# Kernel optimization log

Measured on AMD Instinct MI355X. Metric: run time of the kernel, lower is better.

The kernel has to match this reference:

```python
import jax, jax.numpy as jnp
import numpy as np


def setup_inputs() -> dict:
    key = jax.random.key(0)
    ks = jax.random.split(key, 10)
    B, S, H, I, V = 64, 2048, 512, 512, 50257
    scale = 0.05
    return {
        "last_output": jax.random.randint(ks[0], (B,), 0, V),
        "last_hidden": jax.random.normal(ks[1], (1, B, H), jnp.float32),
        "encoder_outputs": jax.random.normal(ks[2], (S, B, H), jnp.float32),
        "embedding": jax.random.normal(ks[3], (V, I), jnp.float32) * scale,
        "W_ih": jax.random.normal(ks[4], (3 * H, I + H), jnp.float32) * scale,
        "b_ih": jax.random.normal(ks[5], (3 * H,), jnp.float32) * scale,
        "W_hh": jax.random.normal(ks[6], (3 * H, H), jnp.float32) * scale,
        "b_hh": jax.random.normal(ks[7], (3 * H,), jnp.float32) * scale,
        "W_out": jax.random.normal(ks[8], (V, 2 * H), jnp.float32) * scale,
        "b_out": jax.random.normal(ks[9], (V,), jnp.float32) * scale,
    }


def _gru_step(x, h, W_ih, b_ih, W_hh, b_hh):
    # torch nn.GRU parametrization, single layer, single timestep.
    H = h.shape[-1]
    gi = x @ W_ih.T + b_ih  # [B, 3H]
    gh = h @ W_hh.T + b_hh  # [B, 3H]
    i_r, i_z, i_n = gi[:, :H], gi[:, H:2 * H], gi[:, 2 * H:]
    h_r, h_z, h_n = gh[:, :H], gh[:, H:2 * H], gh[:, 2 * H:]
    r = jax.nn.sigmoid(i_r + h_r)
    z = jax.nn.sigmoid(i_z + h_z)
    n = jnp.tanh(i_n + r * h_n)
    return (1.0 - z) * n + z * h


def reference(last_output, last_hidden, encoder_outputs, embedding,
              W_ih, b_ih, W_hh, b_hh, W_out, b_out):
    # Embedding lookup: [B, I]
    embedded = embedding[last_output]
    h_top = last_hidden[-1]  # [B, H]
    # Luong 'dot' attention: score(b, s) = h_b . enc[s, b]
    scores = jnp.einsum('bh,sbh->bs', h_top, encoder_outputs)  # [B, S]
    attn = jax.nn.softmax(scores, axis=-1)                      # [B, S]
    # context = attn @ enc (per batch): [B, H]
    context = jnp.einsum('bs,sbh->bh', attn, encoder_outputs)
    # GRU single step on cat(embedded, context)
    rnn_in = jnp.concatenate([embedded, context], axis=-1)      # [B, I+H]
    h_new = _gru_step(rnn_in, h_top, W_ih, b_ih, W_hh, b_hh)    # [B, H]
    # Output projection on cat(rnn_out, context) -> log_softmax over vocab
    feat = jnp.concatenate([h_new, context], axis=-1)           # [B, 2H]
    logits = feat @ W_out.T + b_out                             # [B, V]
    logp = jax.nn.log_softmax(logits, axis=-1)
    hidden = h_new[None]  # [1, B, H]
    return logp, hidden
```

## Files before the change

### kernel.cpp

```cpp
#include <hip/hip_runtime.h>
#include <hip/hip_bf16.h>
#include <math.h>

#define BB 64
#define SS 2048
#define HH 512
#define VV 50257
#define KD 1024
#define NSPLIT 32
#define NTILE 786

typedef float f32x4 __attribute__((ext_vector_type(4)));
typedef __bf16 bf16x8 __attribute__((ext_vector_type(8)));
typedef __attribute__((address_space(3))) void lds_void;
typedef __attribute__((address_space(1))) const void glb_void;

__device__ __forceinline__ float dot4(float4 a, float4 b) {
  return a.x*b.x + a.y*b.y + a.z*b.z + a.w*b.w;
}

__device__ __forceinline__ bf16x8 cvt8(float4 a, float4 b) {
  bf16x8 r;
  r[0]=(__bf16)a.x; r[1]=(__bf16)a.y; r[2]=(__bf16)a.z; r[3]=(__bf16)a.w;
  r[4]=(__bf16)b.x; r[5]=(__bf16)b.y; r[6]=(__bf16)b.z; r[7]=(__bf16)b.w;
  return r;
}

__device__ __forceinline__ size_t fragAddr(int b, int k) {
  return (size_t)(k >> 5)*2048 + (size_t)(b >> 4)*512
       + (size_t)((k >> 3) & 3)*128 + (size_t)(b & 15)*8 + (size_t)(k & 7);
}

__global__ __launch_bounds__(256) void attn_partial(
    const float* __restrict__ hprev, const float* __restrict__ enc,
    float* __restrict__ pm, float* __restrict__ pl, float* __restrict__ pacc)
{
  const int b = blockIdx.x >> 5;
  const int split = blockIdx.x & 31;
  const int t = threadIdx.x;
  const int w = t >> 6, lane = t & 63;

  const float* hb = hprev + b*HH + lane*8;
  const float4 h0 = *(const float4*)hb;
  const float4 h1 = *(const float4*)(hb + 4);
  const int s0 = split*64 + w*16;

  float m = -INFINITY, lsum = 0.f;
  float acc[8];
#pragma unroll
  for (int j = 0; j < 8; ++j) acc[j] = 0.f;

#pragma unroll 1
  for (int half = 0; half < 2; ++half) {
    float4 ea[8], eb[8];
#pragma unroll
    for (int i = 0; i < 8; ++i) {
      const float* ep = enc + ((size_t)(s0 + half*8 + i)*BB + b)*HH + lane*8;
      ea[i] = *(const float4*)ep; eb[i] = *(const float4*)(ep + 4);
    }
    float dd[8];
#pragma unroll
    for (int i = 0; i < 8; ++i) dd[i] = dot4(h0, ea[i]) + dot4(h1, eb[i]);
#pragma unroll
    for (int off = 32; off >= 1; off >>= 1) {
#pragma unroll
      for (int i = 0; i < 8; ++i) dd[i] += __shfl_xor(dd[i], off, 64);
    }
    float hm = dd[0];
#pragma unroll
    for (int i = 1; i < 8; ++i) hm = fmaxf(hm, dd[i]);
    const float mn = fmaxf(m, hm);
    const float sc = __expf(m - mn);
    float p[8], psum = 0.f;
#pragma unroll
    for (int i = 0; i < 8; ++i) { p[i] = __expf(dd[i] - mn); psum += p[i]; }
    lsum = lsum*sc + psum;
#pragma unroll
    for (int j = 0; j < 8; ++j) acc[j] *= sc;
#pragma unroll
    for (int i = 0; i < 8; ++i) {
      acc[0] += p[i]*ea[i].x; acc[1] += p[i]*ea[i].y;
      acc[2] += p[i]*ea[i].z; acc[3] += p[i]*ea[i].w;
      acc[4] += p[i]*eb[i].x; acc[5] += p[i]*eb[i].y;
      acc[6] += p[i]*eb[i].z; acc[7] += p[i]*eb[i].w;
    }
    m = mn;
  }

  __shared__ float sm4[4], sl4[4];
  __shared__ float sacc[4][HH];
  if (lane == 0) { sm4[w] = m; sl4[w] = lsum; }
  __syncthreads();
  const float M = fmaxf(fmaxf(sm4[0], sm4[1]), fmaxf(sm4[2], sm4[3]));
  const float ew = __expf(m - M);
#pragma unroll
  for (int j = 0; j < 8; ++j) sacc[w][lane*8 + j] = acc[j]*ew;
  __syncthreads();

  const int rec = blockIdx.x;
  for (int hh = t; hh < HH; hh += 256)
    pacc[(size_t)rec*HH + hh] = sacc[0][hh]+sacc[1][hh]+sacc[2][hh]+sacc[3][hh];
  if (t == 0) {
    float L = sl4[0]*__expf(sm4[0]-M) + sl4[1]*__expf(sm4[1]-M)
            + sl4[2]*__expf(sm4[2]-M) + sl4[3]*__expf(sm4[3]-M);
    pm[rec] = M; pl[rec] = L;
  }
}

__global__ __launch_bounds__(256) void attn_reduce(
    const float* __restrict__ pm, const float* __restrict__ pl,
    const float* __restrict__ pacc, __hip_bfloat16* __restrict__ featA)
{
  const int b = blockIdx.x, t = threadIdx.x;
  __shared__ float smm[NSPLIT], sll[NSPLIT], sco[NSPLIT];
  if (t < NSPLIT) { smm[t] = pm[b*NSPLIT + t]; sll[t] = pl[b*NSPLIT + t]; }
  __syncthreads();
  float M = -INFINITY;
  for (int q = 0; q < NSPLIT; ++q) M = fmaxf(M, smm[q]);
  float L = 0.f;
  for (int q = 0; q < NSPLIT; ++q) L += sll[q]*__expf(smm[q]-M);
  const float inv = 1.f/L;
  if (t < NSPLIT) sco[t] = __expf(smm[t]-M)*inv;
  __syncthreads();
  const int hh0 = 2*t;
  float s0 = 0.f, s1 = 0.f;
  for (int q = 0; q < NSPLIT; ++q) {
    const float* pq = pacc + ((size_t)b*NSPLIT + q)*HH;
    s0 += pq[hh0]   * sco[q];
    s1 += pq[hh0+1] * sco[q];
  }
  const size_t a = fragAddr(b, HH + hh0);
  featA[a]   = (__hip_bfloat16)s0;
  featA[a+1] = (__hip_bfloat16)s1;
}

__global__ __launch_bounds__(256) void gru_gemm(
    const int* __restrict__ last_out, const float* __restrict__ emb,
    const float* __restrict__ hprev, const __hip_bfloat16* __restrict__ featA,
    const float* __restrict__ W_ih, const float* __restrict__ W_hh,
    float* __restrict__ gates)
{
  const int u = blockIdx.x;
  const int gt = u / 12;
  const int rem = u % 12;
  const int seg = rem >> 2, ks = rem & 3;
  const int w = threadIdx.x >> 6, lane = threadIdx.x & 63;
  const int col = lane & 15, kg = lane >> 4;
  const int g = gt*64 + w*16 + col;

  const float* wrow = (seg == 2) ? (W_hh + (size_t)g*HH)
                                 : (W_ih + (size_t)g*KD + seg*HH);
  int lo_r[4];
#pragma unroll
  for (int mt = 0; mt < 4; ++mt) lo_r[mt] = last_out[mt*16 + col];

  f32x4 acc[4];
#pragma unroll
  for (int mt = 0; mt < 4; ++mt) acc[mt] = (f32x4){0.f,0.f,0.f,0.f};

  const int kbeg = ks*128, kend = kbeg + 128;
  for (int k0 = kbeg; k0 < kend; k0 += 32) {
    const float* wp = wrow + k0 + kg*8;
    const bf16x8 bf = cvt8(*(const float4*)wp, *(const float4*)(wp+4));
#pragma unroll
    for (int mt = 0; mt < 4; ++mt) {
      const int bb = mt*16 + col;
      bf16x8 af;
      if (seg == 0) {
        const float* ap = emb + (size_t)lo_r[mt]*HH + k0 + kg*8;
        af = cvt8(*(const float4*)ap, *(const float4*)(ap+4));
      } else if (seg == 1) {
        af = *(const bf16x8*)(featA + fragAddr(bb, HH + k0 + kg*8));
      } else {
        const float* ap = hprev + (size_t)bb*HH + k0 + kg*8;
        af = cvt8(*(const float4*)ap, *(const float4*)(ap+4));
      }
      acc[mt] = __builtin_amdgcn_mfma_f32_16x16x32_bf16(af, bf, acc[mt], 0, 0, 0);
    }
  }

  float* gp = gates + (size_t)rem*BB*1536;
#pragma unroll
  for (int mt = 0; mt < 4; ++mt)
#pragma unroll
    for (int reg = 0; reg < 4; ++reg) {
      const int brow = mt*16 + kg*4 + reg;
      gp[(size_t)brow*1536 + g] = acc[mt][reg];
    }
}

__global__ __launch_bounds__(512) void gru_pointwise(
    const float* __restrict__ gates, const float* __restrict__ hprev,
    const float* __restrict__ b_ih, const float* __restrict__ b_hh,
    float* __restrict__ hid_out, __hip_bfloat16* __restrict__ featA)
{
  const int b = blockIdx.x, j = threadIdx.x;

  float i_r = 0.f, i_z = 0.f, i_n = 0.f;
#pragma unroll
  for (int p = 0; p < 8; ++p) {
    const float* gp = gates + ((size_t)p*BB + b)*1536;
    i_r += gp[j]; i_z += gp[HH + j]; i_n += gp[2*HH + j];
  }
  float h_r = 0.f, h_z = 0.f, h_n = 0.f;
#pragma unroll
  for (int p = 8; p < 12; ++p) {
    const float* gp = gates + ((size_t)p*BB + b)*1536;
    h_r += gp[j]; h_z += gp[HH + j]; h_n += gp[2*HH + j];
  }

  const float r = 1.f/(1.f + __expf(-(i_r + h_r + b_ih[j] + b_hh[j])));
  const float z = 1.f/(1.f + __expf(-(i_z + h_z + b_ih[HH+j] + b_hh[HH+j])));
  const float n = tanhf(i_n + b_ih[2*HH+j] + r*(h_n + b_hh[2*HH+j]));
  const float hp = hprev[b*HH + j];
  const float hn = (1.f - z)*n + z*hp;
  hid_out[b*HH + j] = hn;
  featA[fragAddr(b, j)] = (__hip_bfloat16)hn;
}

__global__ __launch_bounds__(256, 6) void logits_gemm(
    const __hip_bfloat16* __restrict__ featA, const float* __restrict__ W_out,
    const float* __restrict__ b_out, float* __restrict__ out,
    float* __restrict__ pmE, float* __restrict__ plE)
{
  __shared__ float smem[4672];
  const int tile = blockIdx.x;
  const int t = threadIdx.x;
  const int w = t >> 6, lane = t & 63;
  const int col = lane & 15, kg = lane >> 4;
  const int vbase = tile*64;
  const int v = vbase + w*16 + col;
  const int rowL = w*16 + col;
  const int sXor = (rowL & 7) << 2;

  const __hip_bfloat16* fp = featA + lane*8;

  auto stage = [&](int buf, int kc) {
#pragma unroll
    for (int i = 0; i < 2; ++i) {
      const int sigma = (w*2 + i)*64 + lane;
      const int row = sigma >> 3;
      const int t16 = sigma & 7;
      const int kdl = (t16*4) ^ ((row & 7) << 2);
      int grow = vbase + row; if (grow > VV-1) grow = VV-1;
      const float* src = W_out + (size_t)grow*KD + kc*32 + kdl;
      __builtin_amdgcn_global_load_lds((glb_void*)src,
          (lds_void*)(smem + buf*2048 + (w*2 + i)*256), 16, 0, 0);
    }
  };

  f32x4 acc[4];
#pragma unroll
  for (int mt = 0; mt < 4; ++mt) acc[mt] = (f32x4){0.f,0.f,0.f,0.f};

  stage(0, 0);
  stage(1, 1);

#pragma unroll 1
  for (int kc = 0; kc < 32; ++kc) {
    if (kc < 31) asm volatile("s_waitcnt vmcnt(2)" ::: "memory");
    else         asm volatile("s_waitcnt vmcnt(0)" ::: "memory");
    __builtin_amdgcn_sched_barrier(0);
    __builtin_amdgcn_s_barrier();

    const float* wt = smem + (kc & 1)*2048;
    const int kin = kg*8;
    const float4 wa = *(const float4*)(wt + rowL*32 + (kin ^ sXor));
    const float4 wb = *(const float4*)(wt + rowL*32 + ((kin + 4) ^ sXor));
    const bf16x8 bf = cvt8(wa, wb);
    const __hip_bfloat16* f = fp + (size_t)kc*2048;
    acc[0] = __builtin_amdgcn_mfma_f32_16x16x32_bf16(*(const bf16x8*)(f),        bf, acc[0], 0, 0, 0);
    acc[1] = __builtin_amdgcn_mfma_f32_16x16x32_bf16(*(const bf16x8*)(f + 512),  bf, acc[1], 0, 0, 0);
    acc[2] = __builtin_amdgcn_mfma_f32_16x16x32_bf16(*(const bf16x8*)(f + 1024), bf, acc[2], 0, 0, 0);
    acc[3] = __builtin_amdgcn_mfma_f32_16x16x32_bf16(*(const bf16x8*)(f + 1536), bf, acc[3], 0, 0, 0);

    __builtin_amdgcn_s_barrier();
    if (kc + 2 < 32) stage(kc & 1, kc + 2);
  }
  __syncthreads();

  float* vals = smem;
  float* pMq = smem + 4160;
  float* pLq = smem + 4416;
  const float bo = (v < VV) ? b_out[v] : 0.f;
#pragma unroll
  for (int mt = 0; mt < 4; ++mt)
#pragma unroll
    for (int reg = 0; reg < 4; ++reg) {
      const float val = acc[mt][reg] + bo;
      const int brow = mt*16 + kg*4 + reg;
      if (v < VV) out[(size_t)brow*VV + v] = val;
      vals[brow*65 + w*16 + col] = (v < VV) ? val : -INFINITY;
    }
  __syncthreads();

  {
    const int row = t & 63, q = t >> 6;
    const float* vr = vals + row*65 + q*16;
    float M = -INFINITY;
#pragma unroll
    for (int i = 0; i < 16; ++i) M = fmaxf(M, vr[i]);
    float L = 0.f;
    if (M > -INFINITY) {
#pragma unroll
      for (int i = 0; i < 16; ++i) L += __expf(vr[i] - M);
    }
    pMq[q*64 + row] = M; pLq[q*64 + row] = L;
  }
  __syncthreads();
  if (t < 64) {
    float M = pMq[t], L = pLq[t];
#pragma unroll
    for (int q = 1; q < 4; ++q) {
      const float mq = pMq[q*64 + t], lq = pLq[q*64 + t];
      if (mq > -INFINITY) {
        const float mn = fmaxf(M, mq);
        L = L*__expf(M - mn) + lq*__expf(mq - mn);
        M = mn;
      }
    }
    pmE[t*1024 + tile] = M; plE[t*1024 + tile] = L;
  }
}

__global__ __launch_bounds__(256) void lsm_sub(
    float* __restrict__ out, const float* __restrict__ pmE,
    const float* __restrict__ plE)
{
  const int t = threadIdx.x;
  const int wv = t >> 6, lane = t & 63;
  const size_t off = (size_t)blockIdx.x * 1024;
  const size_t total = (size_t)BB*VV;
  __shared__ float cs[2];
  __shared__ int rowA_s;

  if (wv < 2) {
    size_t pos = (wv == 0) ? off : (off + 1023 < total ? off + 1023 : total - 1);
    const int row = (int)(pos / VV);
    float M = -INFINITY, L = 0.f;
    for (int q = lane; q < NTILE; q += 64) {
      const float mq = pmE[row*1024 + q], lq = plE[row*1024 + q];
      const float mn = fmaxf(M, mq);
      L = L*__expf(M - mn) + lq*__expf(mq - mn);
      M = mn;
    }
#pragma unroll
    for (int o = 32; o >= 1; o >>= 1) {
      const float m2 = __shfl_xor(M, o, 64), l2 = __shfl_xor(L, o, 64);
      const float mn = fmaxf(M, m2);
      L = L*__expf(M - mn) + l2*__expf(m2 - mn);
      M = mn;
    }
    if (lane == 0) {
      cs[wv] = M + logf(L);
      if (wv == 0) rowA_s = row;
    }
  }
  __syncthreads();

  const size_t i = off + (size_t)t*4;
  if (i >= total) return;
  const size_t rs = (size_t)(rowA_s + 1)*VV;
  float4 v = *(float4*)(out + i);
  v.x -= (i     >= rs) ? cs[1] : cs[0];
  v.y -= (i + 1 >= rs) ? cs[1] : cs[0];
  v.z -= (i + 2 >= rs) ? cs[1] : cs[0];
  v.w -= (i + 3 >= rs) ? cs[1] : cs[0];
  *(float4*)(out + i) = v;
}

extern "C" void kernel_launch(void* const* d_in, const int* in_sizes, int n_in,
                              void* d_out, int out_size, void* d_ws, size_t ws_size,
                              hipStream_t stream)
{
  const int*   last_output = (const int*)d_in[0];
  const float* last_hidden = (const float*)d_in[1];
  const float* enc         = (const float*)d_in[2];
  const float* emb         = (const float*)d_in[3];
  const float* W_ih        = (const float*)d_in[4];
  const float* b_ih        = (const float*)d_in[5];
  const float* W_hh        = (const float*)d_in[6];
  const float* b_hh        = (const float*)d_in[7];
  const float* W_out       = (const float*)d_in[8];
  const float* b_out       = (const float*)d_in[9];
  float* out = (float*)d_out;

  __hip_bfloat16* featA = (__hip_bfloat16*)d_ws;
  float* gates = (float*)((char*)d_ws + 131072);
  float* pm   = gates + (size_t)12*BB*1536;
  float* pl   = pm + BB*NSPLIT;
  float* pmE  = pl + BB*NSPLIT;
  float* plE  = pmE + BB*1024;
  float* pacc = out;
  float* hid_out = out + (size_t)BB*VV;

  attn_partial <<<dim3(BB*NSPLIT), dim3(256), 0, stream>>>(last_hidden, enc, pm, pl, pacc);
  attn_reduce  <<<dim3(BB),        dim3(256), 0, stream>>>(pm, pl, pacc, featA);
  gru_gemm     <<<dim3(24*12),     dim3(256), 0, stream>>>(last_output, emb, last_hidden,
                                                           featA, W_ih, W_hh, gates);
  gru_pointwise<<<dim3(BB),        dim3(512), 0, stream>>>(gates, last_hidden, b_ih, b_hh,
                                                           hid_out, featA);
  logits_gemm  <<<dim3(NTILE),     dim3(256), 0, stream>>>(featA, W_out, b_out, out, pmE, plE);
  lsm_sub      <<<dim3((int)(((size_t)BB*VV + 1023)/1024)), dim3(256), 0, stream>>>(out, pmE, plE);
}
```

Baseline: 156.2 us.

## Halve logits GEMM vocab tile, split batch across waves, triple-buffer W_out

Each logits_gemm block now covers 32 vocab rows instead of 64, which doubles the grid to 1571 blocks. Each wave now owns a 16-row batch slice and computes two 16-column output tiles. W_out staging moves from a double buffer to a three-slot LDS ring with one async load per thread per stage, and the next k-chunk's activation fragment is prefetched into registers. The aim is more blocks in flight to pull W_out harder, plus lower LDS use per block. The cost is twice as many partial max/sum entries for lsm_sub to combine and more repeated featA reads.

```diff
diff --git a/kernel.cpp b/kernel.cpp
--- a/kernel.cpp
+++ b/kernel.cpp
@@ -8,7 +8,7 @@
 #define VV 50257
 #define KD 1024
 #define NSPLIT 32
-#define NTILE 786
+#define NT2 1571
 
 typedef float f32x4 __attribute__((ext_vector_type(4)));
 typedef __bf16 bf16x8 __attribute__((ext_vector_type(8)));
@@ -223,80 +223,80 @@
     const float* __restrict__ b_out, float* __restrict__ out,
     float* __restrict__ pmE, float* __restrict__ plE)
 {
-  __shared__ float smem[4672];
+  __shared__ float smem[3072];
   const int tile = blockIdx.x;
   const int t = threadIdx.x;
   const int w = t >> 6, lane = t & 63;
   const int col = lane & 15, kg = lane >> 4;
-  const int vbase = tile*64;
-  const int v = vbase + w*16 + col;
-  const int rowL = w*16 + col;
-  const int sXor = (rowL & 7) << 2;
-
-  const __hip_bfloat16* fp = featA + lane*8;
+  const int vbase = tile*32;
+
+  const __hip_bfloat16* fp = featA + (size_t)w*512 + lane*8;
 
   auto stage = [&](int buf, int kc) {
-#pragma unroll
-    for (int i = 0; i < 2; ++i) {
-      const int sigma = (w*2 + i)*64 + lane;
-      const int row = sigma >> 3;
-      const int t16 = sigma & 7;
-      const int kdl = (t16*4) ^ ((row & 7) << 2);
-      int grow = vbase + row; if (grow > VV-1) grow = VV-1;
-      const float* src = W_out + (size_t)grow*KD + kc*32 + kdl;
-      __builtin_amdgcn_global_load_lds((glb_void*)src,
-          (lds_void*)(smem + buf*2048 + (w*2 + i)*256), 16, 0, 0);
-    }
+    const int slot = w*64 + lane;
+    const int row = slot >> 3;
+    const int t16 = slot & 7;
+    const int kdl = (t16*4) ^ ((row & 7) << 2);
+    int grow = vbase + row; if (grow > VV-1) grow = VV-1;
+    const float* src = W_out + (size_t)grow*KD + kc*32 + kdl;
+    __builtin_amdgcn_global_load_lds((glb_void*)src,
+        (lds_void*)(smem + buf*1024 + w*256), 16, 0, 0);
   };
 
-  f32x4 acc[4];
-#pragma unroll
-  for (int mt = 0; mt < 4; ++mt) acc[mt] = (f32x4){0.f,0.f,0.f,0.f};
+  f32x4 acc[2];
+  acc[0] = (f32x4){0.f,0.f,0.f,0.f};
+  acc[1] = (f32x4){0.f,0.f,0.f,0.f};
 
   stage(0, 0);
   stage(1, 1);
+  bf16x8 aCur = *(const bf16x8*)(fp);
 
 #pragma unroll 1
   for (int kc = 0; kc < 32; ++kc) {
-    if (kc < 31) asm volatile("s_waitcnt vmcnt(2)" ::: "memory");
+    if (kc < 31) asm volatile("s_waitcnt vmcnt(1)" ::: "memory");
     else         asm volatile("s_waitcnt vmcnt(0)" ::: "memory");
     __builtin_amdgcn_sched_barrier(0);
     __builtin_amdgcn_s_barrier();
 
-    const float* wt = smem + (kc & 1)*2048;
+    const int kn = (kc + 1 < 32) ? kc + 1 : 31;
+    const bf16x8 aNxt = *(const bf16x8*)(fp + (size_t)kn*2048);
+
+    const float* wt = smem + (kc % 3)*1024;
+    const int sX = (col & 7) << 2;
     const int kin = kg*8;
-    const float4 wa = *(const float4*)(wt + rowL*32 + (kin ^ sXor));
-    const float4 wb = *(const float4*)(wt + rowL*32 + ((kin + 4) ^ sXor));
-    const bf16x8 bf = cvt8(wa, wb);
-    const __hip_bfloat16* f = fp + (size_t)kc*2048;
-    acc[0] = __builtin_amdgcn_mfma_f32_16x16x32_bf16(*(const bf16x8*)(f),        bf, acc[0], 0, 0, 0);
-    acc[1] = __builtin_amdgcn_mfma_f32_16x16x32_bf16(*(const bf16x8*)(f + 512),  bf, acc[1], 0, 0, 0);
-    acc[2] = __builtin_amdgcn_mfma_f32_16x16x32_bf16(*(const bf16x8*)(f + 1024), bf, acc[2], 0, 0, 0);
-    acc[3] = __builtin_amdgcn_mfma_f32_16x16x32_bf16(*(const bf16x8*)(f + 1536), bf, acc[3], 0, 0, 0);
+    const float4 w0a = *(const float4*)(wt + col*32 + (kin ^ sX));
+    const float4 w0b = *(const float4*)(wt + col*32 + ((kin + 4) ^ sX));
+    const float4 w1a = *(const float4*)(wt + (16 + col)*32 + (kin ^ sX));
+    const float4 w1b = *(const float4*)(wt + (16 + col)*32 + ((kin + 4) ^ sX));
+    acc[0] = __builtin_amdgcn_mfma_f32_16x16x32_bf16(aCur, cvt8(w0a, w0b), acc[0], 0, 0, 0);
+    acc[1] = __builtin_amdgcn_mfma_f32_16x16x32_bf16(aCur, cvt8(w1a, w1b), acc[1], 0, 0, 0);
 
     __builtin_amdgcn_s_barrier();
-    if (kc + 2 < 32) stage(kc & 1, kc + 2);
+    if (kc + 2 < 32) stage((kc + 2) % 3, kc + 2);
+    aCur = aNxt;
   }
   __syncthreads();
 
   float* vals = smem;
-  float* pMq = smem + 4160;
-  float* pLq = smem + 4416;
-  const float bo = (v < VV) ? b_out[v] : 0.f;
-#pragma unroll
-  for (int mt = 0; mt < 4; ++mt)
+  float* pMq  = smem + 2112;
+  float* pLq  = smem + 2240;
+#pragma unroll
+  for (int ct = 0; ct < 2; ++ct) {
+    const int v = vbase + ct*16 + col;
+    const float bo = (v < VV) ? b_out[v] : 0.f;
 #pragma unroll
     for (int reg = 0; reg < 4; ++reg) {
-      const float val = acc[mt][reg] + bo;
-      const int brow = mt*16 + kg*4 + reg;
+      const int brow = w*16 + kg*4 + reg;
+      const float val = acc[ct][reg] + bo;
       if (v < VV) out[(size_t)brow*VV + v] = val;
-      vals[brow*65 + w*16 + col] = (v < VV) ? val : -INFINITY;
-    }
-  __syncthreads();
-
-  {
+      vals[brow*33 + ct*16 + col] = (v < VV) ? val : -INFINITY;
+    }
+  }
+  __syncthreads();
+
+  if (t < 128) {
     const int row = t & 63, q = t >> 6;
-    const float* vr = vals + row*65 + q*16;
+    const float* vr = vals + row*33 + q*16;
     float M = -INFINITY;
 #pragma unroll
     for (int i = 0; i < 16; ++i) M = fmaxf(M, vr[i]);
@@ -310,16 +310,13 @@
   __syncthreads();
   if (t < 64) {
     float M = pMq[t], L = pLq[t];
-#pragma unroll
-    for (int q = 1; q < 4; ++q) {
-      const float mq = pMq[q*64 + t], lq = pLq[q*64 + t];
-      if (mq > -INFINITY) {
-        const float mn = fmaxf(M, mq);
-        L = L*__expf(M - mn) + lq*__expf(mq - mn);
-        M = mn;
-      }
-    }
-    pmE[t*1024 + tile] = M; plE[t*1024 + tile] = L;
+    const float mq = pMq[64 + t], lq = pLq[64 + t];
+    if (mq > -INFINITY) {
+      const float mn = fmaxf(M, mq);
+      L = L*__expf(M - mn) + lq*__expf(mq - mn);
+      M = mn;
+    }
+    pmE[(size_t)t*2048 + tile] = M; plE[(size_t)t*2048 + tile] = L;
   }
 }
 
@@ -338,8 +335,8 @@
     size_t pos = (wv == 0) ? off : (off + 1023 < total ? off + 1023 : total - 1);
     const int row = (int)(pos / VV);
     float M = -INFINITY, L = 0.f;
-    for (int q = lane; q < NTILE; q += 64) {
-      const float mq = pmE[row*1024 + q], lq = plE[row*1024 + q];
+    for (int q = lane; q < NT2; q += 64) {
+      const float mq = pmE[(size_t)row*2048 + q], lq = plE[(size_t)row*2048 + q];
       const float mn = fmaxf(M, mq);
       L = L*__expf(M - mn) + lq*__expf(mq - mn);
       M = mn;
@@ -390,7 +387,7 @@
   float* pm   = gates + (size_t)12*BB*1536;
   float* pl   = pm + BB*NSPLIT;
   float* pmE  = pl + BB*NSPLIT;
-  float* plE  = pmE + BB*1024;
+  float* plE  = pmE + (size_t)BB*2048;
   float* pacc = out;
   float* hid_out = out + (size_t)BB*VV;
 
@@ -400,6 +397,6 @@
                                                            featA, W_ih, W_hh, gates);
   gru_pointwise<<<dim3(BB),        dim3(512), 0, stream>>>(gates, last_hidden, b_ih, b_hh,
                                                            hid_out, featA);
-  logits_gemm  <<<dim3(NTILE),     dim3(256), 0, stream>>>(featA, W_out, b_out, out, pmE, plE);
+  logits_gemm  <<<dim3(NT2),       dim3(256), 0, stream>>>(featA, W_out, b_out, out, pmE, plE);
   lsm_sub      <<<dim3((int)(((size_t)BB*VV + 1023)/1024)), dim3(256), 0, stream>>>(out, pmE, plE);
 }
```

Measured after the change: 163.8 us. 1.05x slower.
